# Kernel tuning notes

Measured on AMD Instinct MI355X. Metric: run time of the kernel, lower is better.

## Reference

```python
import jax, jax.numpy as jnp
import numpy as np

N_NODES = 16000
N_EDGES = 128000
IN_FEAT = 1024   # nb_iprs
OUT_FEAT = 1024  # RelGraphConv out / embed_dim
N_RELS = 7
NB_GOS = 4096


def setup_inputs() -> dict:
    key = jax.random.key(0)
    ks = jax.random.split(key, 9)
    feat = jax.random.normal(ks[0], (N_NODES, IN_FEAT), dtype=jnp.float32)
    src = jax.random.randint(ks[1], (N_EDGES,), 0, N_NODES, dtype=jnp.int32)
    dst = jax.random.randint(ks[2], (N_EDGES,), 0, N_NODES, dtype=jnp.int32)
    etypes = jax.random.randint(ks[3], (N_EDGES,), 0, N_RELS, dtype=jnp.int32)
    # RelGraphConv params (regularizer=None): per-relation weight, self-loop weight, bias
    s = 1.0 / np.sqrt(IN_FEAT)
    W_rel = jax.random.uniform(ks[4], (N_RELS, IN_FEAT, OUT_FEAT), dtype=jnp.float32, minval=-s, maxval=s)
    W_loop = jax.random.uniform(ks[5], (IN_FEAT, OUT_FEAT), dtype=jnp.float32, minval=-s, maxval=s)
    bias = jnp.zeros((OUT_FEAT,), dtype=jnp.float32)
    # GO embeddings, init U(-k, k) with k = sqrt(1/embed_dim)
    k = 1.0 / np.sqrt(OUT_FEAT)
    go_embed = jax.random.uniform(ks[6], (NB_GOS, OUT_FEAT), dtype=jnp.float32, minval=-k, maxval=k)
    go_rad = jax.random.uniform(ks[7], (NB_GOS, 1), dtype=jnp.float32, minval=-k, maxval=k)
    return {"feat": feat, "src": src, "dst": dst, "etypes": etypes,
            "W_rel": W_rel, "W_loop": W_loop, "bias": bias,
            "go_embed": go_embed, "go_rad": go_rad}


def reference(feat, src, dst, etypes, W_rel, W_loop, bias, go_embed, go_rad):
    n = feat.shape[0]
    # RelGraphConv (sum aggregation, self-loop, bias, no activation):
    # message on edge e: feat[src[e]] @ W_rel[etypes[e]]; by linearity, first
    # segment-sum source features per (dst, rel), then one batched GEMM.
    x_src = feat[src]                                   # [E, in]
    seg = dst.astype(jnp.int32) * N_RELS + etypes       # combined (dst, rel) id
    agg = jax.ops.segment_sum(x_src, seg, num_segments=n * N_RELS)
    agg = agg.reshape(n, N_RELS, IN_FEAT)               # [N, R, in]
    h = jnp.einsum('nri,rio->no', agg, W_rel) + feat @ W_loop + bias  # [N, out]
    # scoring: sigmoid(x @ E_go^T + |rad|)
    logits = jax.nn.sigmoid(h @ go_embed.T + jnp.abs(go_rad).reshape(1, -1))
    return logits
```

## Files before the change

### kernel.cpp

```cpp
#include <hip/hip_runtime.h>
#include <math.h>

#define N_NODES 16000
#define N_EDGES 128000
#define KDIM 1024
#define N_RELS 7
#define NB_GOS 4096
#define KCAT (KDIM * (N_RELS + 1))
#define MPAD 16128

#define BM 128
#define BN 128
#define BK 32
#define CAP2 (N_EDGES + N_RELS * BM)
#define NTILE_E (CAP2 / BM)

typedef __attribute__((ext_vector_type(8))) short bf16x8;
typedef __attribute__((ext_vector_type(8))) unsigned short u16x8;
typedef __attribute__((ext_vector_type(4))) float f32x4;

__device__ __forceinline__ unsigned short f2bf(float f) {
    union { float f; unsigned int u; } v; v.f = f;
    unsigned int u = v.u + 0x7FFFu + ((v.u >> 16) & 1u);
    return (unsigned short)(u >> 16);
}

__device__ __forceinline__ void gload16(const void* g, void* lds) {
    __builtin_amdgcn_global_load_lds(
        (const __attribute__((address_space(1))) unsigned int*)g,
        (__attribute__((address_space(3))) unsigned int*)lds, 16, 0, 0);
}


__global__ __launch_bounds__(256) void conv_bf16(const float* __restrict__ in,
                                                 unsigned short* __restrict__ out, int n8) {
    int i = blockIdx.x * 256 + threadIdx.x;
    if (i >= n8) return;
    const float4* in4 = (const float4*)in;
    float4 x = in4[2 * i], y = in4[2 * i + 1];
    u16x8 o;
    o[0] = f2bf(x.x); o[1] = f2bf(x.y); o[2] = f2bf(x.z); o[3] = f2bf(x.w);
    o[4] = f2bf(y.x); o[5] = f2bf(y.y); o[6] = f2bf(y.z); o[7] = f2bf(y.w);
    *(u16x8*)&out[(size_t)i * 8] = o;
}

__global__ __launch_bounds__(256) void conv_cat(const float* __restrict__ in,
                                                unsigned short* __restrict__ Acat) {
    int i = blockIdx.x * 256 + threadIdx.x;
    if (i >= N_NODES * (KDIM / 8)) return;
    int n = i >> 7, c8 = (i & 127) * 8;
    const float4* in4 = (const float4*)(in + (size_t)n * KDIM + c8);
    float4 x = in4[0], y = in4[1];
    u16x8 o;
    o[0] = f2bf(x.x); o[1] = f2bf(x.y); o[2] = f2bf(x.z); o[3] = f2bf(x.w);
    o[4] = f2bf(y.x); o[5] = f2bf(y.y); o[6] = f2bf(y.z); o[7] = f2bf(y.w);
    *(u16x8*)&Acat[(size_t)n * KCAT + c8] = o;
}

__global__ void transpose_w(const float* __restrict__ Wrel,
                            const float* __restrict__ Wloop,
                            unsigned short* __restrict__ WrelT,
                            unsigned short* __restrict__ WloopT) {
    __shared__ float t[32][33];
    int z = blockIdx.z;
    const float* src = (z < N_RELS) ? Wrel + (size_t)z * KDIM * KDIM : Wloop;
    unsigned short* dst = (z < N_RELS) ? WrelT + (size_t)z * KDIM * KDIM : WloopT;
    int tx = threadIdx.x, ty = threadIdx.y;
    int x = blockIdx.x * 32 + tx;
    int y0 = blockIdx.y * 32;
    #pragma unroll
    for (int j = 0; j < 4; j++)
        t[ty + 8 * j][tx] = src[(size_t)(y0 + ty + 8 * j) * KDIM + x];
    __syncthreads();
    #pragma unroll
    for (int j = 0; j < 4; j++) {
        int n = blockIdx.x * 32 + ty + 8 * j;
        dst[(size_t)n * KDIM + y0 + tx] = f2bf(t[tx][ty + 8 * j]);
    }
}

__global__ void transpose_cat(const float* __restrict__ Wrel,
                              const float* __restrict__ Wloop,
                              unsigned short* __restrict__ BT) {
    __shared__ float t[32][33];
    int z = blockIdx.z;
    const float* src = (z == 0) ? Wloop : Wrel + (size_t)(z - 1) * KDIM * KDIM;
    int tx = threadIdx.x, ty = threadIdx.y;
    int x = blockIdx.x * 32 + tx;
    int y0 = blockIdx.y * 32;
    #pragma unroll
    for (int j = 0; j < 4; j++)
        t[ty + 8 * j][tx] = src[(size_t)(y0 + ty + 8 * j) * KDIM + x];
    __syncthreads();
    #pragma unroll
    for (int j = 0; j < 4; j++) {
        int o = blockIdx.x * 32 + ty + 8 * j;
        BT[(size_t)o * KCAT + z * KDIM + y0 + tx] = f2bf(t[tx][ty + 8 * j]);
    }
}


__global__ void zero_ints(int* p, int n) {
    int i = blockIdx.x * 256 + threadIdx.x;
    if (i < n) p[i] = 0;
}

__global__ void hist_dst(const int* __restrict__ dst, int* cnt) {
    int e = blockIdx.x * 256 + threadIdx.x;
    if (e < N_EDGES) atomicAdd(&cnt[dst[e]], 1);
}

__global__ __launch_bounds__(1024) void scan_offs(const int* __restrict__ cnt,
                                                  int* __restrict__ offs) {
    __shared__ int part[1024];
    int t = threadIdx.x;
    int base = t * 16;
    int local[16];
    int s = 0;
    if (base < N_NODES) {
        #pragma unroll
        for (int j = 0; j < 16; j++) { local[j] = cnt[base + j]; s += local[j]; }
    }
    part[t] = s;
    __syncthreads();
    for (int d = 1; d < 1024; d <<= 1) {
        int v = (t >= d) ? part[t - d] : 0;
        __syncthreads();
        part[t] += v;
        __syncthreads();
    }
    if (base < N_NODES) {
        int ex = (t == 0) ? 0 : part[t - 1];
        #pragma unroll
        for (int j = 0; j < 16; j++) { offs[base + j] = ex; ex += local[j]; }
        if (base + 16 == N_NODES) offs[N_NODES] = ex;
    }
}

__global__ void scatter_dst(const int* __restrict__ src, const int* __restrict__ dst,
                            const int* __restrict__ et, const int* __restrict__ offs,
                            int* cursor, int* __restrict__ se) {
    int e = blockIdx.x * 256 + threadIdx.x;
    if (e < N_EDGES) {
        int d = dst[e];
        int p = atomicAdd(&cursor[d], 1);
        se[offs[d] + p] = (src[e] << 3) | et[e];
    }
}

__global__ __launch_bounds__(256) void aggregate(const float* __restrict__ feat,
                                                 const int* __restrict__ offs,
                                                 const int* __restrict__ se,
                                                 unsigned short* __restrict__ Acat) {
    int n = blockIdx.x;
    int t = threadIdx.x;
    int e0 = offs[n], e1 = offs[n + 1];
    float4 a0 = {0,0,0,0}, a1 = a0, a2 = a0, a3 = a0, a4 = a0, a5 = a0, a6 = a0;
    const float4* f4 = (const float4*)feat;
    for (int i = e0; i < e1; i++) {
        int v = se[i];
        int s = v >> 3, r = v & 7;
        float4 x = f4[(size_t)s * (KDIM / 4) + t];
        #define ADD4(a) { a.x += x.x; a.y += x.y; a.z += x.z; a.w += x.w; }
        switch (r) {
            case 0: ADD4(a0) break; case 1: ADD4(a1) break;
            case 2: ADD4(a2) break; case 3: ADD4(a3) break;
            case 4: ADD4(a4) break; case 5: ADD4(a5) break;
            default: ADD4(a6) break;
        }
        #undef ADD4
    }
    unsigned short* row = Acat + (size_t)n * KCAT + KDIM;
    #define ST4(rr, a) { ushort4 o; o.x = f2bf(a.x); o.y = f2bf(a.y); \
                         o.z = f2bf(a.z); o.w = f2bf(a.w); \
                         *(ushort4*)(row + rr * KDIM + t * 4) = o; }
    ST4(0, a0) ST4(1, a1) ST4(2, a2) ST4(3, a3) ST4(4, a4) ST4(5, a5) ST4(6, a6)
    #undef ST4
}


template<int MODE>
__global__ __launch_bounds__(512, 2) void gemm256(
    const unsigned short* __restrict__ A,
    const unsigned short* __restrict__ BT,
    const float* __restrict__ br,
    void* __restrict__ outv, int kd)
{
    __shared__ unsigned short As[2][256 * 64];
    __shared__ unsigned short Bs[2][256 * 64];

    const int tid = threadIdx.x;
    const int l = tid & 63, w = tid >> 6;
    const int wm = w >> 2, wn = w & 3;
    const int lrow = l & 15, lhi = l >> 4, lx = l & 7;

    const int nwg = gridDim.x * gridDim.y;
    const int b = blockIdx.y * gridDim.x + blockIdx.x;
    const int q8 = nwg >> 3, r8 = nwg & 7;
    const int xcd = b & 7, idx = b >> 3;
    const int wg = (xcd < r8 ? xcd * (q8 + 1) : r8 * (q8 + 1) + (xcd - r8) * q8) + idx;
    const int m0 = (wg / gridDim.x) * 256;
    const int n0 = (wg % gridDim.x) * 256;

    const int NT = kd >> 6;
    const int NI = NT >> 1;

    const int rr = tid >> 3;
    const int cc = (tid & 7) ^ (rr & 7);

    auto stageA = [&](int dbuf, int kt, int half) {
        #pragma unroll
        for (int j = 0; j < 2; j++) {
            unsigned short* lp = &As[dbuf][(size_t)(w * 8 + j * 128 + half * 64) * 64];
            const unsigned short* gp = A + (size_t)(m0 + rr + j * 128 + half * 64) * kd
                                         + kt * 64 + cc * 8;
            gload16(gp, lp);
        }
    };
    auto stageB = [&](int dbuf, int kt, int half) {
        #pragma unroll
        for (int j = 0; j < 2; j++) {
            const int brow = (w & 3) * 8 + (w >> 2) * 64 + j * 128 + half * 32;
            unsigned short* lp = &Bs[dbuf][(size_t)brow * 64];
            const unsigned short* gp = BT + (size_t)(n0 + (rr & 31) + (rr >> 5) * 64
                                                     + j * 128 + half * 32) * kd
                                          + kt * 64 + cc * 8;
            gload16(gp, lp);
        }
    };

    stageA(0, 0, 0); stageB(0, 0, 0); stageA(0, 0, 1); stageB(0, 0, 1);
    stageA(1, 1, 0); stageB(1, 1, 0);
    asm volatile("s_waitcnt vmcnt(4)" ::: "memory");
    __builtin_amdgcn_s_barrier();

    f32x4 acc[8][4] = {};
    bf16x8 afr[4][2], b0[2][2], b1[2][2];

#define LDA(BUF, MH) do { _Pragma("unroll")                                   \
    for (int mi = 0; mi < 4; mi++) { _Pragma("unroll")                        \
        for (int ks = 0; ks < 2; ks++) {                                      \
            const int row_ = wm * 128 + (MH) * 64 + mi * 16 + lrow;           \
            const int ch_ = (ks * 4 + lhi) ^ lx;                              \
            afr[mi][ks] = *(const bf16x8*)&As[BUF][row_ * 64 + ch_ * 8];      \
        } } } while (0)

#define LDB(BUF, NH, DST) do { _Pragma("unroll")                              \
    for (int nj = 0; nj < 2; nj++) { _Pragma("unroll")                        \
        for (int ks = 0; ks < 2; ks++) {                                      \
            const int row_ = wn * 64 + (NH) * 32 + nj * 16 + lrow;            \
            const int ch_ = (ks * 4 + lhi) ^ lx;                              \
            DST[nj][ks] = *(const bf16x8*)&Bs[BUF][row_ * 64 + ch_ * 8];      \
        } } } while (0)

#define MM(MH, NH, BS) do {                                                   \
    __builtin_amdgcn_s_barrier();                                             \
    __builtin_amdgcn_s_setprio(1);                                            \
    _Pragma("unroll")                                                         \
    for (int mi = 0; mi < 4; mi++) { _Pragma("unroll")                        \
        for (int nj = 0; nj < 2; nj++) { _Pragma("unroll")                    \
            for (int ks = 0; ks < 2; ks++)                                    \
                acc[(MH)*4+mi][(NH)*2+nj] = __builtin_amdgcn_mfma_f32_16x16x32_bf16( \
                    afr[mi][ks], BS[nj][ks], acc[(MH)*4+mi][(NH)*2+nj], 0, 0, 0);    \
        } }                                                                   \
    __builtin_amdgcn_s_setprio(0); } while (0)

    for (int t = 0; t < NI; t++) {
        const bool nl = (t + 1 < NI);
        LDA(0, 0); LDB(0, 0, b0);
        stageA(1, 2 * t + 1, 1);
        MM(0, 0, b0);
        __builtin_amdgcn_s_barrier();
        LDB(0, 1, b1);
        stageB(1, 2 * t + 1, 1);
        MM(0, 1, b1);
        __builtin_amdgcn_s_barrier();
        LDA(0, 1);
        if (nl) stageA(0, 2 * t + 2, 0);
        MM(1, 0, b0);
        __builtin_amdgcn_s_barrier();
        if (nl) stageB(0, 2 * t + 2, 0);
        MM(1, 1, b1);
        if (nl) asm volatile("s_waitcnt vmcnt(4)" ::: "memory");
        else    asm volatile("s_waitcnt vmcnt(0)" ::: "memory");
        __builtin_amdgcn_s_barrier();
        LDA(1, 0); LDB(1, 0, b0);
        if (nl) stageA(0, 2 * t + 2, 1);
        MM(0, 0, b0);
        __builtin_amdgcn_s_barrier();
        LDB(1, 1, b1);
        if (nl) stageB(0, 2 * t + 2, 1);
        MM(0, 1, b1);
        __builtin_amdgcn_s_barrier();
        LDA(1, 1);
        if (nl) stageA(1, 2 * t + 3, 0);
        MM(1, 0, b0);
        __builtin_amdgcn_s_barrier();
        if (nl) stageB(1, 2 * t + 3, 0);
        MM(1, 1, b1);
        if (nl) asm volatile("s_waitcnt vmcnt(4)" ::: "memory");
        else    asm volatile("s_waitcnt vmcnt(0)" ::: "memory");
        __builtin_amdgcn_s_barrier();
    }
#undef LDA
#undef LDB
#undef MM

    const int cl = l & 15, rh = (l >> 4) * 4;
    float brv[4];
    #pragma unroll
    for (int nj = 0; nj < 4; nj++) brv[nj] = br[n0 + wn * 64 + nj * 16 + cl];
    #pragma unroll
    for (int mi = 0; mi < 8; mi++) {
        #pragma unroll
        for (int r4 = 0; r4 < 4; r4++) {
            const int row = m0 + wm * 128 + mi * 16 + rh + r4;
            if (MODE == 2 && row >= N_NODES) continue;
            #pragma unroll
            for (int nj = 0; nj < 4; nj++) {
                const int col = n0 + wn * 64 + nj * 16 + cl;
                float x = acc[mi][nj][r4];
                if (MODE == 0) {
                    ((unsigned short*)outv)[(size_t)row * KDIM + col] = f2bf(x + brv[nj]);
                } else {
                    x += fabsf(brv[nj]);
                    ((float*)outv)[(size_t)row * (size_t)NB_GOS + col] =
                        1.0f / (1.0f + __expf(-x));
                }
            }
        }
    }
}


__global__ void init_buckets(int* cnt, int* cursor, int* bucket) {
    int i = blockIdx.x * 256 + threadIdx.x;
    if (i < 8) { cnt[i] = 0; cursor[i] = 0; }
    if (i < CAP2) bucket[i] = -1;
}

__global__ __launch_bounds__(256) void count_etypes(const int* __restrict__ et, int* cnt) {
    __shared__ int lc[N_RELS];
    if (threadIdx.x < N_RELS) lc[threadIdx.x] = 0;
    __syncthreads();
    int e = blockIdx.x * 256 + threadIdx.x;
    if (e < N_EDGES) atomicAdd(&lc[et[e]], 1);
    __syncthreads();
    if (threadIdx.x < N_RELS) atomicAdd(&cnt[threadIdx.x], lc[threadIdx.x]);
}

__global__ void calc_offsets(const int* __restrict__ cnt, int* offs) {
    if (blockIdx.x == 0 && threadIdx.x == 0) {
        int acc = 0;
        offs[0] = 0;
        for (int r = 0; r < N_RELS; r++) {
            acc += ((cnt[r] + BM - 1) / BM) * BM;
            offs[r + 1] = acc;
        }
    }
}

__global__ __launch_bounds__(256) void scatter_edges(const int* __restrict__ et,
                                                     const int* __restrict__ offs,
                                                     int* cursor, int* bucket) {
    __shared__ int lc[N_RELS];
    __shared__ int lbase[N_RELS];
    if (threadIdx.x < N_RELS) lc[threadIdx.x] = 0;
    __syncthreads();
    int e = blockIdx.x * 256 + threadIdx.x;
    int r = 0, my = 0;
    bool valid = (e < N_EDGES);
    if (valid) { r = et[e]; my = atomicAdd(&lc[r], 1); }
    __syncthreads();
    if (threadIdx.x < N_RELS)
        lbase[threadIdx.x] = atomicAdd(&cursor[threadIdx.x], lc[threadIdx.x]);
    __syncthreads();
    if (valid) bucket[offs[r] + lbase[r] + my] = e;
}

template<int MODE>
__global__ __launch_bounds__(256) void mfma_gemm(
    const unsigned short* __restrict__ A,
    const unsigned short* __restrict__ BT,
    const float* __restrict__ br,
    float* __restrict__ out,
    const int* __restrict__ src,
    const int* __restrict__ dst,
    const int* __restrict__ bucket,
    const int* __restrict__ offs,
    int kd)
{
    __shared__ unsigned short As[BM * BK];
    __shared__ unsigned short Bs[BN * BK];
    __shared__ int s_src[BM];
    __shared__ int s_dst[BM];

    const int tid = threadIdx.x;
    const int l = tid & 63;
    const int w = tid >> 6;
    const int wr = w >> 1, wc = w & 1;

    const int nwg = gridDim.x * gridDim.y;
    const int b = blockIdx.y * gridDim.x + blockIdx.x;
    const int cpx = nwg >> 3;
    const int swz = (b & 7) * cpx + (b >> 3);
    const int n0 = (swz / gridDim.y) * BN;
    const int m0 = (swz % gridDim.y) * BM;

    const unsigned short* Bb = BT;
    if (MODE == 1) {
        int rel = -1;
        #pragma unroll
        for (int q = 0; q < N_RELS; q++)
            if (m0 >= offs[q] && m0 < offs[q + 1]) rel = q;
        if (rel < 0) return;
        Bb = BT + (size_t)rel * KDIM * KDIM;
        if (tid < BM) {
            int e = bucket[m0 + tid];
            s_src[tid] = (e >= 0) ? src[e] : -1;
            s_dst[tid] = (e >= 0) ? dst[e] : -1;
        }
        __syncthreads();
    }

    f32x4 acc[4][4] = {};

    const int s0 = tid, s1 = tid + 256;
    const int r0 = s0 >> 2, kc0 = (s0 & 3) * 8;
    const int r1 = s1 >> 2, kc1 = (s1 & 3) * 8;
    unsigned short* ldsA0 = As + (w * 64) * 8;
    unsigned short* ldsA1 = As + (w * 64 + 256) * 8;
    unsigned short* ldsB0 = Bs + (w * 64) * 8;
    unsigned short* ldsB1 = Bs + (w * 64 + 256) * 8;

    size_t arow0, arow1;
    if (MODE == 1) {
        int sr0 = s_src[r0]; arow0 = (sr0 < 0) ? 0 : (size_t)sr0;
        int sr1 = s_src[r1]; arow1 = (sr1 < 0) ? 0 : (size_t)sr1;
    } else {
        arow0 = (size_t)(m0 + r0);
        arow1 = (size_t)(m0 + r1);
    }
    const size_t brow0 = (size_t)(n0 + r0), brow1 = (size_t)(n0 + r1);

    const int fa = (wr * 64 + (l & 15)) * BK + (l >> 4) * 8;
    const int fb = (wc * 64 + (l & 15)) * BK + (l >> 4) * 8;

    for (int k0 = 0; k0 < kd; k0 += BK) {
        gload16(A + arow0 * kd + k0 + kc0, ldsA0);
        gload16(A + arow1 * kd + k0 + kc1, ldsA1);
        gload16(Bb + brow0 * kd + k0 + kc0, ldsB0);
        gload16(Bb + brow1 * kd + k0 + kc1, ldsB1);
        __syncthreads();

        bf16x8 a[4], bfr[4];
        #pragma unroll
        for (int mi = 0; mi < 4; mi++)
            a[mi] = *(const bf16x8*)&As[fa + mi * 16 * BK];
        #pragma unroll
        for (int nj = 0; nj < 4; nj++)
            bfr[nj] = *(const bf16x8*)&Bs[fb + nj * 16 * BK];
        #pragma unroll
        for (int mi = 0; mi < 4; mi++)
            #pragma unroll
            for (int nj = 0; nj < 4; nj++)
                acc[mi][nj] = __builtin_amdgcn_mfma_f32_16x16x32_bf16(a[mi], bfr[nj], acc[mi][nj], 0, 0, 0);
        __syncthreads();
    }

    const int cl = l & 15, rh = (l >> 4) * 4;
    #pragma unroll
    for (int mi = 0; mi < 4; mi++) {
        #pragma unroll
        for (int r4 = 0; r4 < 4; r4++) {
            const int row = wr * 64 + mi * 16 + rh + r4;
            if (MODE == 1) {
                const int d = s_dst[row];
                if (d >= 0) {
                    #pragma unroll
                    for (int nj = 0; nj < 4; nj++) {
                        const int col = n0 + wc * 64 + nj * 16 + cl;
                        atomicAdd(&out[(size_t)d * KDIM + col], acc[mi][nj][r4]);
                    }
                }
            } else if (MODE == 0) {
                #pragma unroll
                for (int nj = 0; nj < 4; nj++) {
                    const int col = n0 + wc * 64 + nj * 16 + cl;
                    out[(size_t)(m0 + row) * KDIM + col] = acc[mi][nj][r4] + br[col];
                }
            } else {
                #pragma unroll
                for (int nj = 0; nj < 4; nj++) {
                    const int col = n0 + wc * 64 + nj * 16 + cl;
                    float x = acc[mi][nj][r4] + fabsf(br[col]);
                    out[(size_t)(m0 + row) * (size_t)NB_GOS + col] = 1.0f / (1.0f + expf(-x));
                }
            }
        }
    }
}


extern "C" void kernel_launch(void* const* d_in, const int* in_sizes, int n_in,
                              void* d_out, int out_size, void* d_ws, size_t ws_size,
                              hipStream_t stream) {
    const float* feat   = (const float*)d_in[0];
    const int*   src    = (const int*)d_in[1];
    const int*   dst    = (const int*)d_in[2];
    const int*   etypes = (const int*)d_in[3];
    const float* W_rel  = (const float*)d_in[4];
    const float* W_loop = (const float*)d_in[5];
    const float* bias   = (const float*)d_in[6];
    const float* go_emb = (const float*)d_in[7];
    const float* go_rad = (const float*)d_in[8];
    float* out = (float*)d_out;

    const size_t ACAT_B = (size_t)MPAD * KCAT * 2;
    const size_t HB_B   = (size_t)MPAD * KDIM * 2;
    const size_t BTC_B  = (size_t)KDIM * KCAT * 2;
    const size_t GOB_B  = (size_t)NB_GOS * KDIM * 2;
    const size_t CNT_B  = 16384 * 4;
    const size_t NEED   = ACAT_B + HB_B + BTC_B + GOB_B + 3 * CNT_B + (size_t)N_EDGES * 4;

    if (ws_size >= NEED) {
        char* p = (char*)d_ws;
        unsigned short* Acat  = (unsigned short*)p;  p += ACAT_B;
        unsigned short* hb    = (unsigned short*)p;  p += HB_B;
        unsigned short* BTcat = (unsigned short*)p;  p += BTC_B;
        unsigned short* gob   = (unsigned short*)p;  p += GOB_B;
        int* cnt    = (int*)p;                       p += CNT_B;
        int* cursor = (int*)p;                       p += CNT_B;
        int* offs   = (int*)p;                       p += CNT_B;
        int* se     = (int*)p;

        zero_ints<<<(2 * 16384 + 255) / 256, 256, 0, stream>>>(cnt, 2 * 16384);
        conv_cat<<<(N_NODES * (KDIM / 8) + 255) / 256, 256, 0, stream>>>(feat, Acat);
        conv_bf16<<<(NB_GOS * KDIM / 8 + 255) / 256, 256, 0, stream>>>(go_emb, gob, NB_GOS * KDIM / 8);
        {
            dim3 g(KDIM / 32, KDIM / 32, N_RELS + 1), bb(32, 8);
            transpose_cat<<<g, bb, 0, stream>>>(W_rel, W_loop, BTcat);
        }
        hist_dst<<<(N_EDGES + 255) / 256, 256, 0, stream>>>(dst, cnt);
        scan_offs<<<1, 1024, 0, stream>>>(cnt, offs);
        scatter_dst<<<(N_EDGES + 255) / 256, 256, 0, stream>>>(src, dst, etypes, offs, cursor, se);
        aggregate<<<N_NODES, 256, 0, stream>>>(feat, offs, se, Acat);

        {
            dim3 g(KDIM / 256, MPAD / 256);
            gemm256<0><<<g, 512, 0, stream>>>(Acat, BTcat, bias, hb, KCAT);
        }
        {
            dim3 g(NB_GOS / 256, MPAD / 256);
            gemm256<2><<<g, 512, 0, stream>>>(hb, gob, go_rad, out, KDIM);
        }
        return;
    }

    char* p = (char*)d_ws;
    float* h            = (float*)p;            p += (size_t)N_NODES * KDIM * 4;
    unsigned short* fb  = (unsigned short*)p;   p += (size_t)N_NODES * KDIM * 2;
    unsigned short* wrT = (unsigned short*)p;   p += (size_t)N_RELS * KDIM * KDIM * 2;
    unsigned short* wlT = (unsigned short*)p;   p += (size_t)KDIM * KDIM * 2;
    unsigned short* gob = (unsigned short*)p;   p += (size_t)NB_GOS * KDIM * 2;
    int* cnt    = (int*)p;
    int* cursor = cnt + 8;
    int* offs   = cursor + 8;
    int* bucket = offs + 16;

    conv_bf16<<<(N_NODES * KDIM / 8 + 255) / 256, 256, 0, stream>>>(feat, fb, N_NODES * KDIM / 8);
    conv_bf16<<<(NB_GOS * KDIM / 8 + 255) / 256, 256, 0, stream>>>(go_emb, gob, NB_GOS * KDIM / 8);
    {
        dim3 g(KDIM / 32, KDIM / 32, N_RELS + 1), bb(32, 8);
        transpose_w<<<g, bb, 0, stream>>>(W_rel, W_loop, wrT, wlT);
    }
    init_buckets<<<(CAP2 + 255) / 256, 256, 0, stream>>>(cnt, cursor, bucket);
    count_etypes<<<(N_EDGES + 255) / 256, 256, 0, stream>>>(etypes, cnt);
    calc_offsets<<<1, 64, 0, stream>>>(cnt, offs);
    scatter_edges<<<(N_EDGES + 255) / 256, 256, 0, stream>>>(etypes, offs, cursor, bucket);
    {
        dim3 g(KDIM / BN, N_NODES / BM);
        mfma_gemm<0><<<g, 256, 0, stream>>>(fb, wlT, bias, h, nullptr, nullptr, nullptr, nullptr, KDIM);
    }
    {
        dim3 g(KDIM / BN, NTILE_E);
        mfma_gemm<1><<<g, 256, 0, stream>>>(fb, wrT, nullptr, h, src, dst, bucket, offs, KDIM);
    }
    conv_bf16<<<(N_NODES * KDIM / 8 + 255) / 256, 256, 0, stream>>>(h, fb, N_NODES * KDIM / 8);
    {
        dim3 g(NB_GOS / BN, N_NODES / BM);
        mfma_gemm<2><<<g, 256, 0, stream>>>(fb, gob, go_rad, out, nullptr, nullptr, nullptr, nullptr, KDIM);
    }
}
```

Before: 646.8 us.

## Merge GEMM sub-phases, make K a template constant, reorder tiles column-major

Each k-tile half now loads both B fragment sets at once and issues all 32 MFMAs per A half in a single block. This halves the number of barriers per iteration and issues the A and B stage loads together. K is now a template parameter and the global pointer bases are hoisted, which simplifies address arithmetic. Workgroups are now mapped M-fastest instead of N-fastest, which changes which B tiles stay hot in L2. Holding b0 and b1 live at the same time raises register pressure and reduces how finely loads are interleaved with compute.

```diff
diff --git a/kernel.cpp b/kernel.cpp
--- a/kernel.cpp
+++ b/kernel.cpp
@@ -179,12 +179,12 @@
 }
 
 
-template<int MODE>
+template<int MODE, int KD>
 __global__ __launch_bounds__(512, 2) void gemm256(
     const unsigned short* __restrict__ A,
     const unsigned short* __restrict__ BT,
     const float* __restrict__ br,
-    void* __restrict__ outv, int kd)
+    void* __restrict__ outv)
 {
     __shared__ unsigned short As[2][256 * 64];
     __shared__ unsigned short Bs[2][256 * 64];
@@ -199,34 +199,28 @@
     const int q8 = nwg >> 3, r8 = nwg & 7;
     const int xcd = b & 7, idx = b >> 3;
     const int wg = (xcd < r8 ? xcd * (q8 + 1) : r8 * (q8 + 1) + (xcd - r8) * q8) + idx;
-    const int m0 = (wg / gridDim.x) * 256;
-    const int n0 = (wg % gridDim.x) * 256;
-
-    const int NT = kd >> 6;
-    const int NI = NT >> 1;
+    const int m0 = (wg % gridDim.y) * 256;
+    const int n0 = (wg / gridDim.y) * 256;
+
+    const int NI = (KD >> 6) >> 1;
 
     const int rr = tid >> 3;
     const int cc = (tid & 7) ^ (rr & 7);
 
+    const unsigned short* gA = A + (size_t)(m0 + rr) * KD + cc * 8;
+    const unsigned short* gB = BT + (size_t)(n0 + (rr & 31) + (rr >> 5) * 64) * KD + cc * 8;
+
     auto stageA = [&](int dbuf, int kt, int half) {
         #pragma unroll
-        for (int j = 0; j < 2; j++) {
-            unsigned short* lp = &As[dbuf][(size_t)(w * 8 + j * 128 + half * 64) * 64];
-            const unsigned short* gp = A + (size_t)(m0 + rr + j * 128 + half * 64) * kd
-                                         + kt * 64 + cc * 8;
-            gload16(gp, lp);
-        }
+        for (int j = 0; j < 2; j++)
+            gload16(gA + (size_t)(j * 128 + half * 64) * KD + kt * 64,
+                    &As[dbuf][(size_t)(w * 8 + j * 128 + half * 64) * 64]);
     };
     auto stageB = [&](int dbuf, int kt, int half) {
         #pragma unroll
-        for (int j = 0; j < 2; j++) {
-            const int brow = (w & 3) * 8 + (w >> 2) * 64 + j * 128 + half * 32;
-            unsigned short* lp = &Bs[dbuf][(size_t)brow * 64];
-            const unsigned short* gp = BT + (size_t)(n0 + (rr & 31) + (rr >> 5) * 64
-                                                     + j * 128 + half * 32) * kd
-                                          + kt * 64 + cc * 8;
-            gload16(gp, lp);
-        }
+        for (int j = 0; j < 2; j++)
+            gload16(gB + (size_t)(j * 128 + half * 32) * KD + kt * 64,
+                    &Bs[dbuf][(size_t)((w & 3) * 8 + (w >> 2) * 64 + j * 128 + half * 32) * 64]);
     };
 
     stageA(0, 0, 0); stageB(0, 0, 0); stageA(0, 0, 1); stageB(0, 0, 1);
@@ -253,58 +247,46 @@
             DST[nj][ks] = *(const bf16x8*)&Bs[BUF][row_ * 64 + ch_ * 8];      \
         } } } while (0)
 
-#define MM(MH, NH, BS) do {                                                   \
+#define MM2(MH) do {                                                          \
     __builtin_amdgcn_s_barrier();                                             \
     __builtin_amdgcn_s_setprio(1);                                            \
     _Pragma("unroll")                                                         \
     for (int mi = 0; mi < 4; mi++) { _Pragma("unroll")                        \
         for (int nj = 0; nj < 2; nj++) { _Pragma("unroll")                    \
-            for (int ks = 0; ks < 2; ks++)                                    \
-                acc[(MH)*4+mi][(NH)*2+nj] = __builtin_amdgcn_mfma_f32_16x16x32_bf16( \
-                    afr[mi][ks], BS[nj][ks], acc[(MH)*4+mi][(NH)*2+nj], 0, 0, 0);    \
-        } }                                                                   \
+            for (int ks = 0; ks < 2; ks++) {                                  \
+                acc[(MH)*4+mi][nj] = __builtin_amdgcn_mfma_f32_16x16x32_bf16( \
+                    afr[mi][ks], b0[nj][ks], acc[(MH)*4+mi][nj], 0, 0, 0);    \
+                acc[(MH)*4+mi][2+nj] = __builtin_amdgcn_mfma_f32_16x16x32_bf16( \
+                    afr[mi][ks], b1[nj][ks], acc[(MH)*4+mi][2+nj], 0, 0, 0);  \
+        } } }                                                                 \
     __builtin_amdgcn_s_setprio(0); } while (0)
 
     for (int t = 0; t < NI; t++) {
         const bool nl = (t + 1 < NI);
-        LDA(0, 0); LDB(0, 0, b0);
-        stageA(1, 2 * t + 1, 1);
-        MM(0, 0, b0);
-        __builtin_amdgcn_s_barrier();
-        LDB(0, 1, b1);
-        stageB(1, 2 * t + 1, 1);
-        MM(0, 1, b1);
+        LDA(0, 0); LDB(0, 0, b0); LDB(0, 1, b1);
+        stageA(1, 2 * t + 1, 1); stageB(1, 2 * t + 1, 1);
+        MM2(0);
         __builtin_amdgcn_s_barrier();
         LDA(0, 1);
-        if (nl) stageA(0, 2 * t + 2, 0);
-        MM(1, 0, b0);
-        __builtin_amdgcn_s_barrier();
-        if (nl) stageB(0, 2 * t + 2, 0);
-        MM(1, 1, b1);
+        if (nl) { stageA(0, 2 * t + 2, 0); stageB(0, 2 * t + 2, 0); }
+        MM2(1);
         if (nl) asm volatile("s_waitcnt vmcnt(4)" ::: "memory");
         else    asm volatile("s_waitcnt vmcnt(0)" ::: "memory");
         __builtin_amdgcn_s_barrier();
-        LDA(1, 0); LDB(1, 0, b0);
-        if (nl) stageA(0, 2 * t + 2, 1);
-        MM(0, 0, b0);
-        __builtin_amdgcn_s_barrier();
-        LDB(1, 1, b1);
-        if (nl) stageB(0, 2 * t + 2, 1);
-        MM(0, 1, b1);
+        LDA(1, 0); LDB(1, 0, b0); LDB(1, 1, b1);
+        if (nl) { stageA(0, 2 * t + 2, 1); stageB(0, 2 * t + 2, 1); }
+        MM2(0);
         __builtin_amdgcn_s_barrier();
         LDA(1, 1);
-        if (nl) stageA(1, 2 * t + 3, 0);
-        MM(1, 0, b0);
-        __builtin_amdgcn_s_barrier();
-        if (nl) stageB(1, 2 * t + 3, 0);
-        MM(1, 1, b1);
+        if (nl) { stageA(1, 2 * t + 3, 0); stageB(1, 2 * t + 3, 0); }
+        MM2(1);
         if (nl) asm volatile("s_waitcnt vmcnt(4)" ::: "memory");
         else    asm volatile("s_waitcnt vmcnt(0)" ::: "memory");
         __builtin_amdgcn_s_barrier();
     }
 #undef LDA
 #undef LDB
-#undef MM
+#undef MM2
 
     const int cl = l & 15, rh = (l >> 4) * 4;
     float brv[4];
@@ -548,11 +530,11 @@
 
         {
             dim3 g(KDIM / 256, MPAD / 256);
-            gemm256<0><<<g, 512, 0, stream>>>(Acat, BTcat, bias, hb, KCAT);
+            gemm256<0, KCAT><<<g, 512, 0, stream>>>(Acat, BTcat, bias, hb);
         }
         {
             dim3 g(NB_GOS / 256, MPAD / 256);
-            gemm256<2><<<g, 512, 0, stream>>>(hb, gob, go_rad, out, KDIM);
+            gemm256<2, KDIM><<<g, 512, 0, stream>>>(hb, gob, go_rad, out);
         }
         return;
     }
```

Result: faster. 619.4 us (-4.2%).
